# Kernel optimization log

Measured on AMD Instinct MI355X. Metric: run time of the kernel, lower is better.

## Reference

```python
import jax, jax.numpy as jnp
import numpy as np


def setup_inputs() -> dict:
    key = jax.random.key(0)
    k1, k2, k3, k4 = jax.random.split(key, 4)
    B, IN, OUT, R = 4096, 4096, 4096, 256
    x = jax.random.normal(k1, (B, IN), dtype=jnp.float32)
    U = jax.random.normal(k2, (R, IN), dtype=jnp.float32) / np.sqrt(IN)
    V = jax.random.normal(k3, (OUT, R), dtype=jnp.float32) / np.sqrt(R)
    bias = jax.random.uniform(k4, (OUT,), dtype=jnp.float32,
                              minval=-IN ** -0.5, maxval=IN ** -0.5)
    return {"x": x, "U": U, "V": V, "bias": bias}


def reference(x, U, V, bias):
    # Low-rank linear: out[b,j] = sum_k V[j,k] * (sum_i U[k,i] * x[b,i]) + bias[j]
    # (the torch loops with sparsity=1.0 / keep_stride==1 compute exactly this)
    t = jnp.einsum('bi,ri->br', x, U)        # [B, R]
    out = jnp.einsum('br,or->bo', t, V) + bias  # [B, OUT]
    return out
```

## Files before the change

kernel.cpp:

```cpp
#include <hip/hip_runtime.h>

typedef __attribute__((ext_vector_type(8))) short bf16x8;
typedef __attribute__((ext_vector_type(4))) float f32x4;

__device__ __forceinline__ unsigned short f2bf(float f) {
  unsigned int u = __float_as_uint(f);
  return (unsigned short)((u + 0x7fffu + ((u >> 16) & 1u)) >> 16);
}

__device__ __forceinline__ float bf2f(unsigned short s) {
  return __uint_as_float(((unsigned int)s) << 16);
}

__device__ __forceinline__ void gload_lds16(const void* g, void* l) {
  __builtin_amdgcn_global_load_lds((const __attribute__((address_space(1))) void*)g,
                                   (__attribute__((address_space(3))) void*)l,
                                   16, 0, 0);
}

__global__ void castUV(const float4* __restrict__ U, const float4* __restrict__ V,
                       ushort4* __restrict__ Ub, ushort4* __restrict__ Vb) {
  const int NU = 256 * 4096 / 4;
  int i = blockIdx.x * 256 + threadIdx.x;
  const float4* s; ushort4* d; int j;
  if (i < NU) { s = U; d = Ub; j = i; }
  else        { s = V; d = Vb; j = i - NU; }
  float4 v = s[j];
  ushort4 o;
  o.x = f2bf(v.x); o.y = f2bf(v.y); o.z = f2bf(v.z); o.w = f2bf(v.w);
  d[j] = o;
}

template <int MREP, int NREP, bool BIAS, bool AFP32, bool OUT_BF16>
__global__ __launch_bounds__(256)
void gemm_nt(const void* __restrict__ Ap,
             const unsigned short* __restrict__ B,
             const float* __restrict__ bias,
             void* __restrict__ Cv,
             int lda, int ldb, int ldc,
             int nkt, int kChunk, long long splitStride) {
  constexpr int BM = 32 * MREP;
  constexpr int BN = 32 * NREP;
  constexpr int ISS_A = BM / 64;
  constexpr int ISS_B = BN / 64;

  __shared__ unsigned short sA[2][BM * 32];
  __shared__ unsigned short sB[2][BN * 32];

  const int tid = threadIdx.x;
  const int l = tid & 63;
  const int w = tid >> 6;
  const int wm = (w >> 1) * (MREP * 16);
  const int wn = (w & 1) * (NREP * 16);
  const int rm = blockIdx.x * BM;
  const int rn = blockIdx.y * BN;
  const int k0base = blockIdx.z * kChunk;

  const int lr = l & 15;
  const int lc8 = (l >> 4) * 8;

  auto stage = [&](int kt, int buf) {
    const int k0 = k0base + kt * 32;
#pragma unroll
    for (int is = 0; is < ISS_B; ++is) {
      int eo = is * 2048 + tid * 8;
      int r = eo >> 5, c = eo & 31;
      gload_lds16(B + (long long)(rn + r) * ldb + k0 + c, &sB[buf][eo]);
    }
    if constexpr (AFP32) {
      const float* A32 = (const float*)Ap;
      constexpr int EPT = BM * 32 / 256;
      const int eo = tid * EPT;
      const int r = eo >> 5, c = eo & 31;
      const float* src = A32 + (long long)(rm + r) * lda + k0 + c;
      if constexpr (EPT == 4) {
        float4 v = *(const float4*)src;
        ushort4 o;
        o.x = f2bf(v.x); o.y = f2bf(v.y); o.z = f2bf(v.z); o.w = f2bf(v.w);
        *(ushort4*)&sA[buf][eo] = o;
      } else {
        float4 v0 = *(const float4*)src;
        float4 v1 = *(const float4*)(src + 4);
        ushort4 o0, o1;
        o0.x = f2bf(v0.x); o0.y = f2bf(v0.y); o0.z = f2bf(v0.z); o0.w = f2bf(v0.w);
        o1.x = f2bf(v1.x); o1.y = f2bf(v1.y); o1.z = f2bf(v1.z); o1.w = f2bf(v1.w);
        *(ushort4*)&sA[buf][eo] = o0;
        *(ushort4*)&sA[buf][eo + 4] = o1;
      }
    } else {
      const unsigned short* A = (const unsigned short*)Ap;
#pragma unroll
      for (int is = 0; is < ISS_A; ++is) {
        int eo = is * 2048 + tid * 8;
        int r = eo >> 5, c = eo & 31;
        gload_lds16(A + (long long)(rm + r) * lda + k0 + c, &sA[buf][eo]);
      }
    }
  };

  f32x4 acc[MREP][NREP] = {};

  stage(0, 0);
  for (int kt = 0; kt < nkt; ++kt) {
    __syncthreads();
    if (kt + 1 < nkt) stage(kt + 1, (kt + 1) & 1);
    const unsigned short* a0 = sA[kt & 1];
    const unsigned short* b0 = sB[kt & 1];
    bf16x8 af[MREP], bfr[NREP];
#pragma unroll
    for (int m = 0; m < MREP; ++m)
      af[m] = *(const bf16x8*)&a0[(wm + m * 16 + lr) * 32 + lc8];
#pragma unroll
    for (int n = 0; n < NREP; ++n)
      bfr[n] = *(const bf16x8*)&b0[(wn + n * 16 + lr) * 32 + lc8];
#pragma unroll
    for (int m = 0; m < MREP; ++m)
#pragma unroll
      for (int n = 0; n < NREP; ++n)
        acc[m][n] = __builtin_amdgcn_mfma_f32_16x16x32_bf16(af[m], bfr[n], acc[m][n], 0, 0, 0);
  }

  const int r0 = rm + wm + (l >> 4) * 4;
  const int c0 = rn + wn + lr;
  if constexpr (OUT_BF16) {
    unsigned short* Cb = (unsigned short*)Cv + (long long)blockIdx.z * splitStride;
#pragma unroll
    for (int n = 0; n < NREP; ++n) {
      const int cc = c0 + n * 16;
#pragma unroll
      for (int m = 0; m < MREP; ++m)
#pragma unroll
        for (int i = 0; i < 4; ++i)
          Cb[(long long)(r0 + m * 16 + i) * ldc + cc] = f2bf(acc[m][n][i]);
    }
  } else {
    float* Cb = (float*)Cv + (long long)blockIdx.z * splitStride;
#pragma unroll
    for (int n = 0; n < NREP; ++n) {
      const int cc = c0 + n * 16;
      const float badd = BIAS ? bias[cc] : 0.0f;
#pragma unroll
      for (int m = 0; m < MREP; ++m)
#pragma unroll
        for (int i = 0; i < 4; ++i)
          Cb[(long long)(r0 + m * 16 + i) * ldc + cc] = acc[m][n][i] + badd;
    }
  }
}

__global__ void reduce8(const ushort4* __restrict__ P, ushort4* __restrict__ t) {
  const int S = 4096 * 256 / 4;
  int i = blockIdx.x * 256 + threadIdx.x;
  float sx = 0, sy = 0, sz = 0, sw = 0;
#pragma unroll
  for (int z = 0; z < 8; ++z) {
    ushort4 v = P[i + z * S];
    sx += bf2f(v.x); sy += bf2f(v.y); sz += bf2f(v.z); sw += bf2f(v.w);
  }
  ushort4 o;
  o.x = f2bf(sx); o.y = f2bf(sy); o.z = f2bf(sz); o.w = f2bf(sw);
  t[i] = o;
}

extern "C" void kernel_launch(void* const* d_in, const int* in_sizes, int n_in,
                              void* d_out, int out_size, void* d_ws, size_t ws_size,
                              hipStream_t stream) {
  const float* x    = (const float*)d_in[0];
  const float* U    = (const float*)d_in[1];
  const float* V    = (const float*)d_in[2];
  const float* bias = (const float*)d_in[3];
  float* out = (float*)d_out;

  char* ws = (char*)d_ws;
  unsigned short* P   = (unsigned short*)ws;
  unsigned short* tb  = (unsigned short*)(ws + (16u << 20));
  unsigned short* Ub  = (unsigned short*)(ws + (18u << 20));
  unsigned short* Vb  = (unsigned short*)(ws + (20u << 20));

  castUV<<<2048, 256, 0, stream>>>((const float4*)U, (const float4*)V,
                                   (ushort4*)Ub, (ushort4*)Vb);

  dim3 g1(4096 / 64, 1, 8);
  gemm_nt<2, 8, false, true, true><<<g1, 256, 0, stream>>>(
      x, Ub, nullptr, P, 4096, 4096, 256,
      16, 512, (long long)4096 * 256);

  reduce8<<<(4096 * 256 / 4) / 256, 256, 0, stream>>>((const ushort4*)P, (ushort4*)tb);

  dim3 g2(4096 / 128, 4096 / 128, 1);
  gemm_nt<4, 4, true, false, false><<<g2, 256, 0, stream>>>(
      tb, Vb, bias, out, 256, 256, 4096,
      8, 0, 0);
}
```

Baseline: 60.84 us.

## Deep-pipeline the first GEMM with register prefetch and multi-buffered LDS

Replaces the generic split-K first GEMM with a dedicated kernel. It keeps four x tiles in flight in registers, holds A in three LDS buffers and U in four, and uses explicit waitcnt and barrier instructions so that global loads run several k-steps ahead of the MFMA work. The goal is to hide the latency of the fp32 x loads, which the previous double-buffered loop exposed on every iteration. The second GEMM template is reduced to its bf16-input, bias form. In exchange the kernel uses more LDS and registers (launch bounds 256,2), and correctness depends on the hand-set vmcnt count.

```diff
diff --git a/kernel.cpp b/kernel.cpp
--- a/kernel.cpp
+++ b/kernel.cpp
@@ -31,14 +31,104 @@
   d[j] = o;
 }
 
-template <int MREP, int NREP, bool BIAS, bool AFP32, bool OUT_BF16>
+template <int NKT>
+__global__ __launch_bounds__(256, 2)
+void gemm1_pipe(const float* __restrict__ x, const unsigned short* __restrict__ U,
+                unsigned short* __restrict__ P) {
+  __shared__ unsigned short sA[3][64 * 32];
+  __shared__ unsigned short sB[4][256 * 32];
+
+  const int tid = threadIdx.x;
+  const int l = tid & 63;
+  const int w = tid >> 6;
+  const int wm = (w >> 1) * 32;
+  const int wn = (w & 1) * 128;
+  const int rm = blockIdx.x * 64;
+  const int k0base = blockIdx.z * (NKT * 32);
+  const int lr = l & 15;
+  const int lc8 = (l >> 4) * 8;
+
+  const float* xs = x + (long long)(rm + (tid >> 2)) * 4096 + k0base + (tid & 3) * 8;
+
+  float4 ar[4][2];
+
+  auto GA = [&](int j, int slot) {
+    const float* s = xs + j * 32;
+    ar[slot][0] = *(const float4*)s;
+    ar[slot][1] = *(const float4*)(s + 4);
+  };
+  auto WR = [&](int jbuf, int slot) {
+    float4 v0 = ar[slot][0], v1 = ar[slot][1];
+    ushort4 o0, o1;
+    o0.x = f2bf(v0.x); o0.y = f2bf(v0.y); o0.z = f2bf(v0.z); o0.w = f2bf(v0.w);
+    o1.x = f2bf(v1.x); o1.y = f2bf(v1.y); o1.z = f2bf(v1.z); o1.w = f2bf(v1.w);
+    ushort4* d = (ushort4*)&sA[jbuf % 3][tid * 8];
+    d[0] = o0; d[1] = o1;
+  };
+  auto GB = [&](int jdata, int jbuf) {
+    const int k0 = k0base + jdata * 32;
+#pragma unroll
+    for (int is = 0; is < 4; ++is) {
+      int eo = is * 2048 + tid * 8;
+      gload_lds16(U + (long long)(eo >> 5) * 4096 + k0 + (eo & 31),
+                  &sB[jbuf % 4][eo]);
+    }
+  };
+
+  f32x4 acc[2][8] = {};
+
+  GA(0, 0); GA(1, 1); GA(2, 2);
+  GB(0, 0);
+  GA(3, 3);
+  GB(1, 1);
+  WR(0, 0);
+
+#pragma unroll
+  for (int j = 0; j < NKT; ++j) {
+    GA((j + 4 < NKT) ? (j + 4) : (NKT - 1), (j + 4) & 3);
+    WR(j + 1, (j + 1) & 3);
+    GB((j + 2 < NKT) ? (j + 2) : (NKT - 1), j + 2);
+    asm volatile("s_waitcnt vmcnt(12) lgkmcnt(0)" ::: "memory");
+    __builtin_amdgcn_sched_barrier(0);
+    __builtin_amdgcn_s_barrier();
+    __builtin_amdgcn_sched_barrier(0);
+    const unsigned short* a0 = sA[j % 3];
+    const unsigned short* b0 = sB[j % 4];
+    bf16x8 af[2], bf[8];
+#pragma unroll
+    for (int m = 0; m < 2; ++m)
+      af[m] = *(const bf16x8*)&a0[(wm + m * 16 + lr) * 32 + lc8];
+#pragma unroll
+    for (int n = 0; n < 8; ++n)
+      bf[n] = *(const bf16x8*)&b0[(wn + n * 16 + lr) * 32 + lc8];
+#pragma unroll
+    for (int m = 0; m < 2; ++m)
+#pragma unroll
+      for (int n = 0; n < 8; ++n)
+        acc[m][n] = __builtin_amdgcn_mfma_f32_16x16x32_bf16(af[m], bf[n], acc[m][n], 0, 0, 0);
+  }
+
+  unsigned short* Cb = P + (long long)blockIdx.z * (4096LL * 256);
+  const int r0 = rm + wm + (l >> 4) * 4;
+  const int c0 = wn + lr;
+#pragma unroll
+  for (int n = 0; n < 8; ++n) {
+    const int cc = c0 + n * 16;
+#pragma unroll
+    for (int m = 0; m < 2; ++m)
+#pragma unroll
+      for (int i = 0; i < 4; ++i)
+        Cb[(long long)(r0 + m * 16 + i) * 256 + cc] = f2bf(acc[m][n][i]);
+  }
+}
+
+template <int MREP, int NREP>
 __global__ __launch_bounds__(256)
-void gemm_nt(const void* __restrict__ Ap,
+void gemm_nt(const unsigned short* __restrict__ A,
              const unsigned short* __restrict__ B,
              const float* __restrict__ bias,
-             void* __restrict__ Cv,
-             int lda, int ldb, int ldc,
-             int nkt, int kChunk, long long splitStride) {
+             float* __restrict__ C,
+             int lda, int ldb, int ldc, int nkt) {
   constexpr int BM = 32 * MREP;
   constexpr int BN = 32 * NREP;
   constexpr int ISS_A = BM / 64;
@@ -54,47 +144,23 @@
   const int wn = (w & 1) * (NREP * 16);
   const int rm = blockIdx.x * BM;
   const int rn = blockIdx.y * BN;
-  const int k0base = blockIdx.z * kChunk;
 
   const int lr = l & 15;
   const int lc8 = (l >> 4) * 8;
 
   auto stage = [&](int kt, int buf) {
-    const int k0 = k0base + kt * 32;
+    const int k0 = kt * 32;
 #pragma unroll
     for (int is = 0; is < ISS_B; ++is) {
       int eo = is * 2048 + tid * 8;
       int r = eo >> 5, c = eo & 31;
       gload_lds16(B + (long long)(rn + r) * ldb + k0 + c, &sB[buf][eo]);
     }
-    if constexpr (AFP32) {
-      const float* A32 = (const float*)Ap;
-      constexpr int EPT = BM * 32 / 256;
-      const int eo = tid * EPT;
-      const int r = eo >> 5, c = eo & 31;
-      const float* src = A32 + (long long)(rm + r) * lda + k0 + c;
-      if constexpr (EPT == 4) {
-        float4 v = *(const float4*)src;
-        ushort4 o;
-        o.x = f2bf(v.x); o.y = f2bf(v.y); o.z = f2bf(v.z); o.w = f2bf(v.w);
-        *(ushort4*)&sA[buf][eo] = o;
-      } else {
-        float4 v0 = *(const float4*)src;
-        float4 v1 = *(const float4*)(src + 4);
-        ushort4 o0, o1;
-        o0.x = f2bf(v0.x); o0.y = f2bf(v0.y); o0.z = f2bf(v0.z); o0.w = f2bf(v0.w);
-        o1.x = f2bf(v1.x); o1.y = f2bf(v1.y); o1.z = f2bf(v1.z); o1.w = f2bf(v1.w);
-        *(ushort4*)&sA[buf][eo] = o0;
-        *(ushort4*)&sA[buf][eo + 4] = o1;
-      }
-    } else {
-      const unsigned short* A = (const unsigned short*)Ap;
-#pragma unroll
-      for (int is = 0; is < ISS_A; ++is) {
-        int eo = is * 2048 + tid * 8;
-        int r = eo >> 5, c = eo & 31;
-        gload_lds16(A + (long long)(rm + r) * lda + k0 + c, &sA[buf][eo]);
-      }
+#pragma unroll
+    for (int is = 0; is < ISS_A; ++is) {
+      int eo = is * 2048 + tid * 8;
+      int r = eo >> 5, c = eo & 31;
+      gload_lds16(A + (long long)(rm + r) * lda + k0 + c, &sA[buf][eo]);
     }
   };
 
@@ -122,29 +188,15 @@
 
   const int r0 = rm + wm + (l >> 4) * 4;
   const int c0 = rn + wn + lr;
-  if constexpr (OUT_BF16) {
-    unsigned short* Cb = (unsigned short*)Cv + (long long)blockIdx.z * splitStride;
-#pragma unroll
-    for (int n = 0; n < NREP; ++n) {
-      const int cc = c0 + n * 16;
-#pragma unroll
-      for (int m = 0; m < MREP; ++m)
-#pragma unroll
-        for (int i = 0; i < 4; ++i)
-          Cb[(long long)(r0 + m * 16 + i) * ldc + cc] = f2bf(acc[m][n][i]);
-    }
-  } else {
-    float* Cb = (float*)Cv + (long long)blockIdx.z * splitStride;
-#pragma unroll
-    for (int n = 0; n < NREP; ++n) {
-      const int cc = c0 + n * 16;
-      const float badd = BIAS ? bias[cc] : 0.0f;
-#pragma unroll
-      for (int m = 0; m < MREP; ++m)
-#pragma unroll
-        for (int i = 0; i < 4; ++i)
-          Cb[(long long)(r0 + m * 16 + i) * ldc + cc] = acc[m][n][i] + badd;
-    }
+#pragma unroll
+  for (int n = 0; n < NREP; ++n) {
+    const int cc = c0 + n * 16;
+    const float badd = bias[cc];
+#pragma unroll
+    for (int m = 0; m < MREP; ++m)
+#pragma unroll
+      for (int i = 0; i < 4; ++i)
+        C[(long long)(r0 + m * 16 + i) * ldc + cc] = acc[m][n][i] + badd;
   }
 }
 
@@ -181,14 +233,10 @@
                                    (ushort4*)Ub, (ushort4*)Vb);
 
   dim3 g1(4096 / 64, 1, 8);
-  gemm_nt<2, 8, false, true, true><<<g1, 256, 0, stream>>>(
-      x, Ub, nullptr, P, 4096, 4096, 256,
-      16, 512, (long long)4096 * 256);
+  gemm1_pipe<16><<<g1, 256, 0, stream>>>(x, Ub, P);
 
   reduce8<<<(4096 * 256 / 4) / 256, 256, 0, stream>>>((const ushort4*)P, (ushort4*)tb);
 
   dim3 g2(4096 / 128, 4096 / 128, 1);
-  gemm_nt<4, 4, true, false, false><<<g2, 256, 0, stream>>>(
-      tb, Vb, bias, out, 256, 256, 4096,
-      8, 0, 0);
-}
+  gemm_nt<4, 4><<<g2, 256, 0, stream>>>(tb, Vb, bias, out, 256, 256, 4096, 8);
+}
```

New measurement: 57.06 us. -6.2%, faster.

## Load fp32 x tiles directly to LDS and double split-K factor

Applied to the files above, without the earlier changes.

The first GEMM now streams fp32 x tiles straight into LDS with async global-to-LDS loads and converts them to bf16 when reading fragments, instead of loading through registers and converting before the LDS store. Split-K for the first GEMM goes from 8 to 16 chunks, giving more blocks for parallelism, with a 16-way reduction kernel and a larger partial buffer in the workspace. The change doubles LDS footprint for A and repeats the conversion per wave. It also doubles partial-sum traffic through the reduction.

```diff
diff --git a/kernel.cpp b/kernel.cpp
--- a/kernel.cpp
+++ b/kernel.cpp
@@ -41,10 +41,10 @@
              int nkt, int kChunk, long long splitStride) {
   constexpr int BM = 32 * MREP;
   constexpr int BN = 32 * NREP;
-  constexpr int ISS_A = BM / 64;
+  constexpr int AELT = AFP32 ? 4 : 2;
   constexpr int ISS_B = BN / 64;
 
-  __shared__ unsigned short sA[2][BM * 32];
+  __shared__ __align__(16) char sA[2][BM * 32 * AELT];
   __shared__ unsigned short sB[2][BN * 32];
 
   const int tid = threadIdx.x;
@@ -64,36 +64,24 @@
 #pragma unroll
     for (int is = 0; is < ISS_B; ++is) {
       int eo = is * 2048 + tid * 8;
-      int r = eo >> 5, c = eo & 31;
-      gload_lds16(B + (long long)(rn + r) * ldb + k0 + c, &sB[buf][eo]);
+      gload_lds16(B + (long long)(rn + (eo >> 5)) * ldb + k0 + (eo & 31),
+                  &sB[buf][eo]);
     }
     if constexpr (AFP32) {
       const float* A32 = (const float*)Ap;
-      constexpr int EPT = BM * 32 / 256;
-      const int eo = tid * EPT;
-      const int r = eo >> 5, c = eo & 31;
-      const float* src = A32 + (long long)(rm + r) * lda + k0 + c;
-      if constexpr (EPT == 4) {
-        float4 v = *(const float4*)src;
-        ushort4 o;
-        o.x = f2bf(v.x); o.y = f2bf(v.y); o.z = f2bf(v.z); o.w = f2bf(v.w);
-        *(ushort4*)&sA[buf][eo] = o;
-      } else {
-        float4 v0 = *(const float4*)src;
-        float4 v1 = *(const float4*)(src + 4);
-        ushort4 o0, o1;
-        o0.x = f2bf(v0.x); o0.y = f2bf(v0.y); o0.z = f2bf(v0.z); o0.w = f2bf(v0.w);
-        o1.x = f2bf(v1.x); o1.y = f2bf(v1.y); o1.z = f2bf(v1.z); o1.w = f2bf(v1.w);
-        *(ushort4*)&sA[buf][eo] = o0;
-        *(ushort4*)&sA[buf][eo + 4] = o1;
+#pragma unroll
+      for (int is = 0; is < BM * 32 / 1024; ++is) {
+        int fo = is * 1024 + tid * 4;
+        gload_lds16(A32 + (long long)(rm + (fo >> 5)) * lda + k0 + (fo & 31),
+                    (float*)sA[buf] + fo);
       }
     } else {
       const unsigned short* A = (const unsigned short*)Ap;
 #pragma unroll
-      for (int is = 0; is < ISS_A; ++is) {
+      for (int is = 0; is < BM / 64; ++is) {
         int eo = is * 2048 + tid * 8;
-        int r = eo >> 5, c = eo & 31;
-        gload_lds16(A + (long long)(rm + r) * lda + k0 + c, &sA[buf][eo]);
+        gload_lds16(A + (long long)(rm + (eo >> 5)) * lda + k0 + (eo & 31),
+                    (unsigned short*)sA[buf] + eo);
       }
     }
   };
@@ -104,15 +92,30 @@
   for (int kt = 0; kt < nkt; ++kt) {
     __syncthreads();
     if (kt + 1 < nkt) stage(kt + 1, (kt + 1) & 1);
-    const unsigned short* a0 = sA[kt & 1];
-    const unsigned short* b0 = sB[kt & 1];
     bf16x8 af[MREP], bfr[NREP];
+    if constexpr (AFP32) {
+      const float* a0 = (const float*)sA[kt & 1];
 #pragma unroll
-    for (int m = 0; m < MREP; ++m)
-      af[m] = *(const bf16x8*)&a0[(wm + m * 16 + lr) * 32 + lc8];
+      for (int m = 0; m < MREP; ++m) {
+        const float* p = a0 + (wm + m * 16 + lr) * 32 + lc8;
+        float4 u0 = *(const float4*)p;
+        float4 u1 = *(const float4*)(p + 4);
+        bf16x8 t;
+        t[0] = (short)f2bf(u0.x); t[1] = (short)f2bf(u0.y);
+        t[2] = (short)f2bf(u0.z); t[3] = (short)f2bf(u0.w);
+        t[4] = (short)f2bf(u1.x); t[5] = (short)f2bf(u1.y);
+        t[6] = (short)f2bf(u1.z); t[7] = (short)f2bf(u1.w);
+        af[m] = t;
+      }
+    } else {
+      const unsigned short* a0 = (const unsigned short*)sA[kt & 1];
+#pragma unroll
+      for (int m = 0; m < MREP; ++m)
+        af[m] = *(const bf16x8*)&a0[(wm + m * 16 + lr) * 32 + lc8];
+    }
 #pragma unroll
     for (int n = 0; n < NREP; ++n)
-      bfr[n] = *(const bf16x8*)&b0[(wn + n * 16 + lr) * 32 + lc8];
+      bfr[n] = *(const bf16x8*)&sB[kt & 1][(wn + n * 16 + lr) * 32 + lc8];
 #pragma unroll
     for (int m = 0; m < MREP; ++m)
 #pragma unroll
@@ -148,12 +151,12 @@
   }
 }
 
-__global__ void reduce8(const ushort4* __restrict__ P, ushort4* __restrict__ t) {
+__global__ void reduce16(const ushort4* __restrict__ P, ushort4* __restrict__ t) {
   const int S = 4096 * 256 / 4;
   int i = blockIdx.x * 256 + threadIdx.x;
   float sx = 0, sy = 0, sz = 0, sw = 0;
 #pragma unroll
-  for (int z = 0; z < 8; ++z) {
+  for (int z = 0; z < 16; ++z) {
     ushort4 v = P[i + z * S];
     sx += bf2f(v.x); sy += bf2f(v.y); sz += bf2f(v.z); sw += bf2f(v.w);
   }
@@ -173,19 +176,19 @@
 
   char* ws = (char*)d_ws;
   unsigned short* P   = (unsigned short*)ws;
-  unsigned short* tb  = (unsigned short*)(ws + (16u << 20));
-  unsigned short* Ub  = (unsigned short*)(ws + (18u << 20));
-  unsigned short* Vb  = (unsigned short*)(ws + (20u << 20));
+  unsigned short* tb  = (unsigned short*)(ws + (32u << 20));
+  unsigned short* Ub  = (unsigned short*)(ws + (34u << 20));
+  unsigned short* Vb  = (unsigned short*)(ws + (36u << 20));
 
   castUV<<<2048, 256, 0, stream>>>((const float4*)U, (const float4*)V,
                                    (ushort4*)Ub, (ushort4*)Vb);
 
-  dim3 g1(4096 / 64, 1, 8);
+  dim3 g1(4096 / 64, 1, 16);
   gemm_nt<2, 8, false, true, true><<<g1, 256, 0, stream>>>(
       x, Ub, nullptr, P, 4096, 4096, 256,
-      16, 512, (long long)4096 * 256);
+      8, 256, (long long)4096 * 256);
 
-  reduce8<<<(4096 * 256 / 4) / 256, 256, 0, stream>>>((const ushort4*)P, (ushort4*)tb);
+  reduce16<<<(4096 * 256 / 4) / 256, 256, 0, stream>>>((const ushort4*)P, (ushort4*)tb);
 
   dim3 g2(4096 / 128, 4096 / 128, 1);
   gemm_nt<4, 4, true, false, false><<<g2, 256, 0, stream>>>(
```

After: 63.94 us. +5.1%, slower.
